# Performance work log

Hardware: AMD Instinct MI355X
Metric: run time of the kernel (lower is better)

The kernel has to match this reference:

```python
import jax, jax.numpy as jnp
import numpy as np

N = 50000      # users
F_IN = 768     # input features
H = 128        # hidden_dimension == linear_channels
E = 400000     # edges per relation
SQRT_D = float(np.sqrt(H))  # heads=1 -> d = H


def leaky_relu(x):
    return jnp.where(x >= 0, x, 0.01 * x)


def hgt_layer(x, edge_list, Wk, bk, Wq, bq, Wv, bv, rel_params, Wa, ba, skip):
    # x: [N, H]; edge_list: list of [2, E] int arrays (row0=src, row1=dst)
    n = x.shape[0]
    k = x @ Wk + bk
    q = x @ Wq + bq
    v = x @ Wv + bv
    out = jnp.zeros_like(x)
    for ei, (A, M, p) in zip(edge_list, rel_params):
        src, dst = ei[0], ei[1]
        kr = (k @ A)[src]                                  # [E, H] gather
        vr = (v @ M)[src]                                  # [E, H] gather
        alpha = jnp.sum(q[dst] * kr, axis=-1) * p[0] / SQRT_D  # [E]
        amax = jax.ops.segment_max(alpha, dst, num_segments=n)
        ex = jnp.exp(alpha - amax[dst])
        denom = jax.ops.segment_sum(ex, dst, num_segments=n)
        w = ex / denom[dst]                                # segment softmax per dst
        out = out + jax.ops.segment_sum(vr * w[:, None], dst, num_segments=n)
    out = jax.nn.gelu(out, approximate=False) @ Wa + ba
    beta = jax.nn.sigmoid(skip[0])                          # learnable skip gate
    return beta * out + (1.0 - beta) * x


def setup_inputs() -> dict:
    key = jax.random.key(0)
    ks = jax.random.split(key, 16)
    d = {}
    d['features'] = jax.random.normal(ks[0], (N, F_IN), dtype=jnp.float32)
    d['edge_index0'] = jax.random.randint(ks[1], (2, E), 0, N, dtype=jnp.int64)
    d['edge_index1'] = jax.random.randint(ks[2], (2, E), 0, N, dtype=jnp.int64)
    d['W1'] = jax.random.normal(ks[3], (F_IN, H), dtype=jnp.float32) / np.sqrt(F_IN)
    d['b1'] = jnp.zeros((H,), jnp.float32)
    d['Wk'] = jax.random.normal(ks[4], (H, H), dtype=jnp.float32) / np.sqrt(H)
    d['bk'] = jnp.zeros((H,), jnp.float32)
    d['Wq'] = jax.random.normal(ks[5], (H, H), dtype=jnp.float32) / np.sqrt(H)
    d['bq'] = jnp.zeros((H,), jnp.float32)
    d['Wv'] = jax.random.normal(ks[6], (H, H), dtype=jnp.float32) / np.sqrt(H)
    d['bv'] = jnp.zeros((H,), jnp.float32)
    d['A0'] = jax.random.normal(ks[7], (H, H), dtype=jnp.float32) / np.sqrt(H)
    d['M0'] = jax.random.normal(ks[8], (H, H), dtype=jnp.float32) / np.sqrt(H)
    d['p0'] = jnp.ones((1,), jnp.float32)
    d['A1'] = jax.random.normal(ks[9], (H, H), dtype=jnp.float32) / np.sqrt(H)
    d['M1'] = jax.random.normal(ks[10], (H, H), dtype=jnp.float32) / np.sqrt(H)
    d['p1'] = jnp.ones((1,), jnp.float32)
    d['Wa'] = jax.random.normal(ks[11], (H, H), dtype=jnp.float32) / np.sqrt(H)
    d['ba'] = jnp.zeros((H,), jnp.float32)
    d['skip'] = jnp.ones((1,), jnp.float32)
    d['Wo1'] = jax.random.normal(ks[12], (H, 64), dtype=jnp.float32) / np.sqrt(H)
    d['bo1'] = jnp.zeros((64,), jnp.float32)
    d['Wo2'] = jax.random.normal(ks[13], (64, 2), dtype=jnp.float32) / np.sqrt(64)
    d['bo2'] = jnp.zeros((2,), jnp.float32)
    return d


def reference(features, edge_index0, edge_index1, W1, b1, Wk, bk, Wq, bq, Wv, bv,
              A0, M0, p0, A1, M1, p1, Wa, ba, skip, Wo1, bo1, Wo2, bo2):
    edges = [edge_index0, edge_index1]
    rel_params = [(A0, M0, p0), (A1, M1, p1)]
    # linear1 + LeakyReLU (dropout is identity in eval mode)
    x = leaky_relu(features @ W1 + b1)
    # HGT_layer1 applied twice (as in the original forward)
    x = hgt_layer(x, edges, Wk, bk, Wq, bq, Wv, bv, rel_params, Wa, ba, skip)
    x = hgt_layer(x, edges, Wk, bk, Wq, bq, Wv, bv, rel_params, Wa, ba, skip)
    x = leaky_relu(x @ Wo1 + bo1)
    return x @ Wo2 + bo2
```

## Files before the change

### kernel.cpp

```cpp
#include <hip/hip_runtime.h>
#include <math.h>

#define NNODES 50000
#define FIN 768
#define HDIM 128
#define NEDGE 400000
#define NSB 49

typedef _Float16 half8 __attribute__((ext_vector_type(8)));
typedef _Float16 half4 __attribute__((ext_vector_type(4)));
typedef _Float16 half2v __attribute__((ext_vector_type(2)));
typedef float f32x4 __attribute__((ext_vector_type(4)));

__device__ __forceinline__ void gld_lds16(const void* g, void* l) {
    __builtin_amdgcn_global_load_lds((const __attribute__((address_space(1))) unsigned int*)g,
                                     (__attribute__((address_space(3))) unsigned int*)l, 16, 0, 0);
}


__global__ __launch_bounds__(256) void count2_kernel(const int* __restrict__ ei0, const int* __restrict__ ei1,
                                                     int* __restrict__ deg0, int* __restrict__ deg1) {
    int e = blockIdx.x * 256 + threadIdx.x;
    const int* ei = blockIdx.y ? ei1 : ei0;
    int* deg = blockIdx.y ? deg1 : deg0;
    if (e < NEDGE) atomicAdd(&deg[ei[NEDGE + e]], 1);
}

__global__ __launch_bounds__(1024) void scan1_kernel(const int* __restrict__ deg0, const int* __restrict__ deg1,
                                                     int* __restrict__ ptr0, int* __restrict__ ptr1,
                                                     int* __restrict__ sums) {
    const int r = blockIdx.y;
    const int* deg = r ? deg1 : deg0;
    int* ptr = r ? ptr1 : ptr0;
    const int b = blockIdx.x, t = threadIdx.x, i = b * 1024 + t;
    __shared__ int buf[1024];
    int v = (i < NNODES) ? deg[i] : 0;
    buf[t] = v;
    __syncthreads();
    for (int off = 1; off < 1024; off <<= 1) {
        int x = (t >= off) ? buf[t - off] : 0;
        __syncthreads();
        buf[t] += x;
        __syncthreads();
    }
    if (i < NNODES) ptr[i] = buf[t] - v;
    if (t == 1023) sums[r * 64 + b] = buf[1023];
}

__global__ __launch_bounds__(64) void scan2_kernel(int* __restrict__ sums,
                                                   int* __restrict__ ptr0, int* __restrict__ ptr1) {
    const int r = blockIdx.x, t = threadIdx.x;
    int orig = (t < NSB) ? sums[r * 64 + t] : 0;
    int v = orig;
    #pragma unroll
    for (int off = 1; off < 64; off <<= 1) {
        int u = __shfl_up(v, off, 64);
        if (t >= off) v += u;
    }
    if (t < NSB) sums[r * 64 + t] = v - orig;
    if (t == NSB - 1) (r ? ptr1 : ptr0)[NNODES] = v;
}

__global__ __launch_bounds__(1024) void scan3_kernel(const int* __restrict__ sums,
                                                     int* __restrict__ ptr0, int* __restrict__ ptr1) {
    const int r = blockIdx.y;
    int* ptr = r ? ptr1 : ptr0;
    const int i = blockIdx.x * 1024 + threadIdx.x;
    if (i < NNODES) ptr[i] += sums[r * 64 + blockIdx.x];
}

__global__ __launch_bounds__(256) void scatter2_kernel(const int* __restrict__ ei0, const int* __restrict__ ei1,
                                                       const int* __restrict__ ptr0, const int* __restrict__ ptr1,
                                                       int* __restrict__ fill0, int* __restrict__ fill1,
                                                       int* __restrict__ csr0, int* __restrict__ csr1) {
    int e = blockIdx.x * 256 + threadIdx.x;
    const int* ei = blockIdx.y ? ei1 : ei0;
    const int* ptr = blockIdx.y ? ptr1 : ptr0;
    int* fill = blockIdx.y ? fill1 : fill0;
    int* csr = blockIdx.y ? csr1 : csr0;
    if (e < NEDGE) {
        int s = ei[e], d = ei[NEDGE + e];
        int p = atomicAdd(&fill[d], 1);
        csr[ptr[d] + p] = s;
    }
}

__global__ __launch_bounds__(256) void gemm_cmb_kernel(
    const float* __restrict__ Wk, const float* __restrict__ Wv,
    const float* __restrict__ A0v, const float* __restrict__ M0v,
    const float* __restrict__ A1v, const float* __restrict__ M1v,
    float* __restrict__ WkA0, float* __restrict__ WvM0,
    float* __restrict__ WkA1, float* __restrict__ WvM1)
{
    const int z = blockIdx.z;
    const float* A = (z & 1) ? Wv : Wk;
    const float* B = (z == 0) ? A0v : (z == 1) ? M0v : (z == 2) ? A1v : M1v;
    float* C = (z == 0) ? WkA0 : (z == 1) ? WvM0 : (z == 2) ? WkA1 : WvM1;
    const int M = 128, N = 128, K = 128;
    __shared__ float As[16][64];
    __shared__ float Bs[16][64];
    const int t = threadIdx.x;
    const int tx = t & 15, ty = t >> 4;
    const int bm = blockIdx.x * 64, bn = blockIdx.y * 64;
    const int ar = t >> 2, ac = (t & 3) << 2;
    const int br = t >> 4, bc = (t & 15) << 2;
    float acc[4][4] = {};
    for (int kb = 0; kb < K; kb += 16) {
        float4 av = *reinterpret_cast<const float4*>(A + (size_t)(bm + ar) * K + kb + ac);
        float4 bv = *reinterpret_cast<const float4*>(B + (size_t)(kb + br) * N + bn + bc);
        __syncthreads();
        As[ac + 0][ar] = av.x; As[ac + 1][ar] = av.y; As[ac + 2][ar] = av.z; As[ac + 3][ar] = av.w;
        *reinterpret_cast<float4*>(&Bs[br][bc]) = bv;
        __syncthreads();
        #pragma unroll
        for (int kk = 0; kk < 16; ++kk) {
            float4 a = *reinterpret_cast<const float4*>(&As[kk][ty << 2]);
            float4 b = *reinterpret_cast<const float4*>(&Bs[kk][tx << 2]);
            float am[4] = {a.x, a.y, a.z, a.w};
            float bb[4] = {b.x, b.y, b.z, b.w};
            #pragma unroll
            for (int i = 0; i < 4; ++i)
                #pragma unroll
                for (int j = 0; j < 4; ++j)
                    acc[i][j] = fmaf(am[i], bb[j], acc[i][j]);
        }
    }
    #pragma unroll
    for (int i = 0; i < 4; ++i)
        #pragma unroll
        for (int j = 0; j < 4; ++j)
            C[(size_t)(bm + (ty << 2) + i) * N + bn + (tx << 2) + j] = acc[i][j];
}

__global__ __launch_bounds__(128) void bias_cmb_kernel(
    const float* __restrict__ bk, const float* __restrict__ bv,
    const float* __restrict__ A0v, const float* __restrict__ M0v,
    const float* __restrict__ A1v, const float* __restrict__ M1v,
    float* __restrict__ bqkv)
{
    const int z = blockIdx.x;
    const int j = threadIdx.x;
    const float* b = (z & 1) ? bv : bk;
    const float* Mtx = (z == 0) ? A0v : (z == 1) ? M0v : (z == 2) ? A1v : M1v;
    float s = 0.f;
    for (int i = 0; i < HDIM; ++i) s += b[i] * Mtx[i * HDIM + j];
    const int r = z >> 1, kv = z & 1;
    bqkv[128 + r * 256 + ((j >> 1) << 2) + (kv << 1) + (j & 1)] = s;
}

__global__ __launch_bounds__(128) void pack_qkvT(
    const float* __restrict__ Wq,   const float* __restrict__ WkA0, const float* __restrict__ WvM0,
    const float* __restrict__ WkA1, const float* __restrict__ WvM1,
    const float* __restrict__ bq,
    _Float16* __restrict__ WT, float* __restrict__ bb)
{
    int n = blockIdx.x;
    int k = threadIdx.x;
    int seg = n >> 7, col = n & 127;
    const float* W = (seg == 0) ? Wq : (seg == 1) ? WkA0 : (seg == 2) ? WvM0 : (seg == 3) ? WkA1 : WvM1;
    int np;
    if (seg == 0) np = col;
    else {
        int r = (seg - 1) >> 1, kv = (seg - 1) & 1;
        np = 128 + r * 256 + ((col >> 1) << 2) + (kv << 1) + (col & 1);
    }
    WT[(size_t)np * 128 + k] = (_Float16)W[(size_t)k * 128 + col];
    if (seg == 0 && k == 0) bb[col] = bq[col];
}

__global__ void transpose_h(const float* __restrict__ W, _Float16* __restrict__ WT, int K, int N) {
    int n = blockIdx.x, k = threadIdx.x;
    WT[(size_t)n * K + k] = (_Float16)W[(size_t)k * N + n];
}

template<int MODE, bool A_F32, bool GELU>
__global__ __launch_bounds__(256) void gemm_h(
    const void* __restrict__ Av, const _Float16* __restrict__ Bt,
    const float* __restrict__ bias, const _Float16* __restrict__ Dh,
    const float* __restrict__ gate, _Float16* __restrict__ C,
    int M, int N, int K)
{
    __shared__ _Float16 sA[4096];
    __shared__ _Float16 sB[4096];
    const int t = threadIdx.x;
    const int w = t >> 6, lane = t & 63;
    const int wm = w >> 1, wn = w & 1;
    const int bm = blockIdx.x * 128, bn = blockIdx.y * 128;
    const f32x4 zero = {0.f, 0.f, 0.f, 0.f};
    f32x4 acc[4][4];
    #pragma unroll
    for (int i = 0; i < 4; ++i)
        #pragma unroll
        for (int j = 0; j < 4; ++j) acc[i][j] = zero;

    for (int kb = 0; kb < K; kb += 32) {
        #pragma unroll
        for (int it = 0; it < 2; ++it) {
            const int c = it * 256 + t;
            const int l = c & 63;
            const int row = ((c >> 6) << 4) | (l & 15);
            const int kc = (l >> 4) << 3;
            const int cb = it * 256 + (t & 192);
            int arow = bm + row; if (arow > M - 1) arow = M - 1;
            int brow = bn + row; if (brow > N - 1) brow = N - 1;
            if (A_F32) {
                const float* ap = (const float*)Av + (size_t)arow * K + kb + kc;
                f32x4 v0 = *(const f32x4*)ap;
                f32x4 v1 = *(const f32x4*)(ap + 4);
                float tmp[8] = {v0[0], v0[1], v0[2], v0[3], v1[0], v1[1], v1[2], v1[3]};
                half8 av;
                #pragma unroll
                for (int j = 0; j < 8; ++j) {
                    float x = tmp[j];
                    if (GELU) x = 0.5f * x * (1.0f + erff(x * 0.70710678118654752f));
                    av[j] = (_Float16)x;
                }
                *(half8*)(sA + (size_t)c * 8) = av;
            } else {
                gld_lds16((const _Float16*)Av + (size_t)arow * K + kb + kc, sA + (size_t)cb * 8);
            }
            gld_lds16(Bt + (size_t)brow * K + kb + kc, sB + (size_t)cb * 8);
        }
        __syncthreads();
        half8 af[4], bf[4];
        #pragma unroll
        for (int i = 0; i < 4; ++i) af[i] = *(const half8*)(sA + ((size_t)((wm * 4 + i) * 64 + lane)) * 8);
        #pragma unroll
        for (int i = 0; i < 4; ++i) bf[i] = *(const half8*)(sB + ((size_t)((wn * 4 + i) * 64 + lane)) * 8);
        #pragma unroll
        for (int i = 0; i < 4; ++i)
            #pragma unroll
            for (int j = 0; j < 4; ++j)
                acc[i][j] = __builtin_amdgcn_mfma_f32_16x16x32_f16(af[i], bf[j], acc[i][j], 0, 0, 0);
        __syncthreads();
    }

    float be = 0.f;
    if (MODE == 2) be = 1.0f / (1.0f + __expf(-gate[0]));
    const int crow0 = bm + wm * 64;
    const int ccol0 = bn + wn * 64;
    #pragma unroll
    for (int i = 0; i < 4; ++i) {
        #pragma unroll
        for (int j = 0; j < 4; ++j) {
            const int col = ccol0 + j * 16 + (lane & 15);
            if (col >= N) continue;
            #pragma unroll
            for (int r = 0; r < 4; ++r) {
                const int row = crow0 + i * 16 + ((lane >> 4) << 2) + r;
                if (row >= M) continue;
                float val = acc[i][j][r] + bias[col];
                if (MODE == 1) val = (val >= 0.f) ? val : 0.01f * val;
                if (MODE == 2) val = be * val + (1.f - be) * (float)Dh[(size_t)row * HDIM + col];
                C[(size_t)row * N + col] = (_Float16)val;
            }
        }
    }
}

template<int MODE, bool A_F32, bool GELU>
__global__ __launch_bounds__(256) void gemm_h32(
    const void* __restrict__ Av, const _Float16* __restrict__ Bt,
    const float* __restrict__ bias, const _Float16* __restrict__ Dh,
    const float* __restrict__ gate, _Float16* __restrict__ C,
    int M, int N, int K)
{
    __shared__ _Float16 sA[4 * 64 * 8];
    __shared__ _Float16 sB[16 * 64 * 8];
    const int t = threadIdx.x;
    const int w = t >> 6, lane = t & 63;
    const int rl = lane & 15, kg = lane >> 4;
    const int bm = blockIdx.x * 32;
    const f32x4 zero = {0.f, 0.f, 0.f, 0.f};
    f32x4 acc[2][2] = {{zero, zero}, {zero, zero}};

    for (int kb = 0; kb < K; kb += 64) {
        {
            const int mi = w >> 1, kk = w & 1;
            int arow = bm + mi * 16 + rl; if (arow > M - 1) arow = M - 1;
            const int ko = kb + kk * 32 + kg * 8;
            if (A_F32) {
                const float* ap = (const float*)Av + (size_t)arow * K + ko;
                f32x4 v0 = *(const f32x4*)ap;
                f32x4 v1 = *(const f32x4*)(ap + 4);
                float tmp[8] = {v0[0], v0[1], v0[2], v0[3], v1[0], v1[1], v1[2], v1[3]};
                half8 av;
                #pragma unroll
                for (int j = 0; j < 8; ++j) {
                    float x = tmp[j];
                    if (GELU) x = 0.5f * x * (1.0f + erff(x * 0.70710678118654752f));
                    av[j] = (_Float16)x;
                }
                *(half8*)(sA + (size_t)(w * 64 + lane) * 8) = av;
            } else {
                gld_lds16((const _Float16*)Av + (size_t)arow * K + ko, sA + (size_t)(w * 64) * 8);
            }
        }
        #pragma unroll
        for (int j = 0; j < 4; ++j) {
            const int fb = w * 4 + j;
            const int ni = (j >> 1) & 1, kk = j & 1;
            int nrow = w * 32 + ni * 16 + rl; if (nrow > N - 1) nrow = N - 1;
            gld_lds16(Bt + (size_t)nrow * K + kb + kk * 32 + kg * 8, sB + (size_t)(fb * 64) * 8);
        }
        __syncthreads();
        half8 af[2][2], bf[2][2];
        #pragma unroll
        for (int mi = 0; mi < 2; ++mi)
            #pragma unroll
            for (int kk = 0; kk < 2; ++kk)
                af[mi][kk] = *(const half8*)(sA + (size_t)((mi * 2 + kk) * 64 + lane) * 8);
        #pragma unroll
        for (int ni = 0; ni < 2; ++ni)
            #pragma unroll
            for (int kk = 0; kk < 2; ++kk)
                bf[ni][kk] = *(const half8*)(sB + (size_t)((w * 4 + ni * 2 + kk) * 64 + lane) * 8);
        #pragma unroll
        for (int mi = 0; mi < 2; ++mi)
            #pragma unroll
            for (int ni = 0; ni < 2; ++ni)
                #pragma unroll
                for (int kk = 0; kk < 2; ++kk)
                    acc[mi][ni] = __builtin_amdgcn_mfma_f32_16x16x32_f16(af[mi][kk], bf[ni][kk], acc[mi][ni], 0, 0, 0);
        __syncthreads();
    }

    float be = 0.f;
    if (MODE == 2) be = 1.0f / (1.0f + __expf(-gate[0]));
    #pragma unroll
    for (int mi = 0; mi < 2; ++mi) {
        #pragma unroll
        for (int ni = 0; ni < 2; ++ni) {
            const int col = w * 32 + ni * 16 + rl;
            if (col >= N) continue;
            #pragma unroll
            for (int r = 0; r < 4; ++r) {
                const int row = bm + mi * 16 + kg * 4 + r;
                if (row >= M) continue;
                float val = acc[mi][ni][r] + bias[col];
                if (MODE == 1) val = (val >= 0.f) ? val : 0.01f * val;
                if (MODE == 2) val = be * val + (1.f - be) * (float)Dh[(size_t)row * HDIM + col];
                C[(size_t)row * N + col] = (_Float16)val;
            }
        }
    }
}

__global__ __launch_bounds__(256) void attn2_kernel(
    const _Float16* __restrict__ qkv,
    const int* __restrict__ ptr0, const int* __restrict__ csr0,
    const int* __restrict__ ptr1, const int* __restrict__ csr1,
    const float* __restrict__ p0, const float* __restrict__ p1,
    float* __restrict__ att)
{
    const int w = (blockIdx.x * 256 + threadIdx.x) >> 6;
    if (w >= NNODES) return;
    const int lane = threadIdx.x & 63;
    half2v qh = *(const half2v*)(qkv + (size_t)w * 640 + (lane << 1));
    const float qx = (float)qh[0], qy = (float)qh[1];
    float ox = 0.f, oy = 0.f;
    #pragma unroll
    for (int r = 0; r < 2; ++r) {
        const int* ptrv = r ? ptr1 : ptr0;
        const int* csr  = r ? csr1 : csr0;
        const float scale = (r ? p1[0] : p0[0]) * 0.08838834764831845f;
        const int start = ptrv[w], end = ptrv[w + 1];
        if (start == end) continue;
        const _Float16* tbl = qkv + 128 + 256 * r + (lane << 2);
        float denom = 0.f, ax = 0.f, ay = 0.f;
        int i = start;
        for (; i + 4 <= end; i += 4) {
            const int s0 = csr[i], s1 = csr[i + 1], s2 = csr[i + 2], s3 = csr[i + 3];
            half4 kv0 = *(const half4*)(tbl + (size_t)s0 * 640);
            half4 kv1 = *(const half4*)(tbl + (size_t)s1 * 640);
            half4 kv2 = *(const half4*)(tbl + (size_t)s2 * 640);
            half4 kv3 = *(const half4*)(tbl + (size_t)s3 * 640);
            float d0 = qx * (float)kv0[0] + qy * (float)kv0[1];
            float d1 = qx * (float)kv1[0] + qy * (float)kv1[1];
            float d2 = qx * (float)kv2[0] + qy * (float)kv2[1];
            float d3 = qx * (float)kv3[0] + qy * (float)kv3[1];
            #pragma unroll
            for (int o2 = 32; o2; o2 >>= 1) {
                d0 += __shfl_xor(d0, o2, 64);
                d1 += __shfl_xor(d1, o2, 64);
                d2 += __shfl_xor(d2, o2, 64);
                d3 += __shfl_xor(d3, o2, 64);
            }
            const float e0 = __expf(d0 * scale), e1 = __expf(d1 * scale);
            const float e2 = __expf(d2 * scale), e3 = __expf(d3 * scale);
            denom += (e0 + e1) + (e2 + e3);
            ax += e0 * (float)kv0[2] + e1 * (float)kv1[2] + e2 * (float)kv2[2] + e3 * (float)kv3[2];
            ay += e0 * (float)kv0[3] + e1 * (float)kv1[3] + e2 * (float)kv2[3] + e3 * (float)kv3[3];
        }
        for (; i < end; ++i) {
            const int s = csr[i];
            half4 kv = *(const half4*)(tbl + (size_t)s * 640);
            float d = qx * (float)kv[0] + qy * (float)kv[1];
            #pragma unroll
            for (int o2 = 32; o2; o2 >>= 1) d += __shfl_xor(d, o2, 64);
            const float e = __expf(d * scale);
            denom += e;
            ax += e * (float)kv[2];
            ay += e * (float)kv[3];
        }
        const float inv = 1.0f / denom;
        ox += ax * inv; oy += ay * inv;
    }
    *reinterpret_cast<float2*>(att + (size_t)w * HDIM + (lane << 1)) = make_float2(ox, oy);
}

__global__ __launch_bounds__(256) void head2_kernel(const _Float16* __restrict__ h,
                                                    const float* __restrict__ Wo2,
                                                    const float* __restrict__ bo2,
                                                    float* __restrict__ out)
{
    int i = blockIdx.x * 256 + threadIdx.x;
    if (i >= NNODES) return;
    const _Float16* hp = h + (size_t)i * 64;
    float s0 = bo2[0], s1 = bo2[1];
    #pragma unroll
    for (int j0 = 0; j0 < 64; j0 += 8) {
        half8 hv = *(const half8*)(hp + j0);
        #pragma unroll
        for (int j = 0; j < 8; ++j) {
            float v = (float)hv[j];
            s0 += v * Wo2[2 * (j0 + j)];
            s1 += v * Wo2[2 * (j0 + j) + 1];
        }
    }
    out[2 * i] = s0;
    out[2 * i + 1] = s1;
}


extern "C" void kernel_launch(void* const* d_in, const int* in_sizes, int n_in,
                              void* d_out, int out_size, void* d_ws, size_t ws_size,
                              hipStream_t stream)
{
    const float* features = (const float*)d_in[0];
    const int* ei0 = (const int*)d_in[1];
    const int* ei1 = (const int*)d_in[2];
    const float* W1 = (const float*)d_in[3];
    const float* b1 = (const float*)d_in[4];
    const float* Wk = (const float*)d_in[5];
    const float* bk = (const float*)d_in[6];
    const float* Wq = (const float*)d_in[7];
    const float* bq = (const float*)d_in[8];
    const float* Wv = (const float*)d_in[9];
    const float* bv = (const float*)d_in[10];
    const float* A0 = (const float*)d_in[11];
    const float* M0 = (const float*)d_in[12];
    const float* p0 = (const float*)d_in[13];
    const float* A1 = (const float*)d_in[14];
    const float* M1 = (const float*)d_in[15];
    const float* p1 = (const float*)d_in[16];
    const float* Wa = (const float*)d_in[17];
    const float* ba = (const float*)d_in[18];
    const float* skip = (const float*)d_in[19];
    const float* Wo1 = (const float*)d_in[20];
    const float* bo1 = (const float*)d_in[21];
    const float* Wo2 = (const float*)d_in[22];
    const float* bo2 = (const float*)d_in[23];
    (void)in_sizes; (void)n_in; (void)out_size; (void)ws_size;

    char* base = (char*)d_ws;
    size_t off = 0;
    auto alloc = [&](size_t bytes) { size_t r = off; off = (off + bytes + 255) & ~(size_t)255; return base + r; };

    _Float16* x0h  = (_Float16*)alloc((size_t)NNODES * HDIM * 2);
    _Float16* x1h  = (_Float16*)alloc((size_t)NNODES * HDIM * 2);
    _Float16* qkv  = (_Float16*)alloc((size_t)NNODES * 640 * 2);
    float*    att  = (float*)   alloc((size_t)NNODES * HDIM * 4);
    _Float16* hh   = (_Float16*)alloc((size_t)NNODES * 64 * 2);
    float* WkA[2]  = { (float*)alloc(65536), (float*)alloc(65536) };
    float* WvM[2]  = { (float*)alloc(65536), (float*)alloc(65536) };
    _Float16* WqkvT = (_Float16*)alloc(640 * 128 * 2);
    float*    bqkv  = (float*)   alloc(640 * 4);
    _Float16* W1T   = (_Float16*)alloc(128 * 768 * 2);
    _Float16* WaT   = (_Float16*)alloc(128 * 128 * 2);
    _Float16* Wo1T  = (_Float16*)alloc(64 * 128 * 2);
    int* deg[2]  = { (int*)alloc(NNODES * 4), (int*)alloc(NNODES * 4) };
    int* ptrv[2] = { (int*)alloc((NNODES + 1) * 4), (int*)alloc((NNODES + 1) * 4) };
    int* fill[2] = { (int*)alloc(NNODES * 4), (int*)alloc(NNODES * 4) };
    int* csr[2]  = { (int*)alloc(NEDGE * 4),  (int*)alloc(NEDGE * 4) };
    int* sums    = (int*)alloc(2 * 64 * 4);

    hipMemsetAsync(deg[0], 0, NNODES * 4, stream);
    hipMemsetAsync(deg[1], 0, NNODES * 4, stream);
    hipMemsetAsync(fill[0], 0, NNODES * 4, stream);
    hipMemsetAsync(fill[1], 0, NNODES * 4, stream);
    const int egrid = (NEDGE + 255) / 256;
    count2_kernel<<<dim3(egrid, 2), 256, 0, stream>>>(ei0, ei1, deg[0], deg[1]);
    scan1_kernel<<<dim3(NSB, 2), 1024, 0, stream>>>(deg[0], deg[1], ptrv[0], ptrv[1], sums);
    scan2_kernel<<<2, 64, 0, stream>>>(sums, ptrv[0], ptrv[1]);
    scan3_kernel<<<dim3(NSB, 2), 1024, 0, stream>>>(sums, ptrv[0], ptrv[1]);
    scatter2_kernel<<<dim3(egrid, 2), 256, 0, stream>>>(ei0, ei1, ptrv[0], ptrv[1],
                                                        fill[0], fill[1], csr[0], csr[1]);

    gemm_cmb_kernel<<<dim3(2, 2, 4), 256, 0, stream>>>(Wk, Wv, A0, M0, A1, M1,
                                                       WkA[0], WvM[0], WkA[1], WvM[1]);
    bias_cmb_kernel<<<4, 128, 0, stream>>>(bk, bv, A0, M0, A1, M1, bqkv);

    pack_qkvT<<<640, 128, 0, stream>>>(Wq, WkA[0], WvM[0], WkA[1], WvM[1], bq, WqkvT, bqkv);
    transpose_h<<<128, 768, 0, stream>>>(W1, W1T, 768, 128);
    transpose_h<<<128, 128, 0, stream>>>(Wa, WaT, 128, 128);
    transpose_h<<<64, 128, 0, stream>>>(Wo1, Wo1T, 128, 64);

    const int MBLK = (NNODES + 127) / 128;
    const int MBLK32 = (NNODES + 31) / 32;

    gemm_h32<1, true, false><<<MBLK32, 256, 0, stream>>>(
        features, W1T, b1, nullptr, nullptr, x0h, NNODES, HDIM, FIN);

    _Float16* xin = x0h;
    _Float16* xout = x1h;
    for (int layer = 0; layer < 2; ++layer) {
        gemm_h<0, false, false><<<dim3(MBLK, 5), 256, 0, stream>>>(
            xin, WqkvT, bqkv, nullptr, nullptr, qkv, NNODES, 640, HDIM);
        attn2_kernel<<<(NNODES * 64 + 255) / 256, 256, 0, stream>>>(
            qkv, ptrv[0], csr[0], ptrv[1], csr[1], p0, p1, att);
        gemm_h32<2, true, true><<<MBLK32, 256, 0, stream>>>(
            att, WaT, ba, xin, skip, xout, NNODES, HDIM, HDIM);
        _Float16* tmp = xin; xin = xout; xout = tmp;
    }

    gemm_h32<1, false, false><<<MBLK32, 256, 0, stream>>>(
        xin, Wo1T, bo1, nullptr, nullptr, hh, NNODES, 64, HDIM);
    head2_kernel<<<(NNODES + 255) / 256, 256, 0, stream>>>(hh, Wo2, bo2, (float*)d_out);
}
```

Measured before the change: 482.3 us.

## Double-buffer LDS tiles in GEMM kernels to overlap loads with MFMA

Both GEMM kernels now keep two LDS buffers. The loads for the next K tile are issued before the MFMAs on the current tile, and only one barrier runs per iteration. For fp32 A inputs the values are held in registers across the MFMA block and converted (with optional GELU) into the other buffer afterwards. This is meant to hide global-load latency behind compute, at the cost of double the LDS footprint and more live registers, which may lower occupancy.

New measurement: 495.1 us. 2.7% more time.

```diff
diff --git a/kernel.cpp b/kernel.cpp
--- a/kernel.cpp
+++ b/kernel.cpp
@@ -15,6 +15,19 @@
 __device__ __forceinline__ void gld_lds16(const void* g, void* l) {
     __builtin_amdgcn_global_load_lds((const __attribute__((address_space(1))) unsigned int*)g,
                                      (__attribute__((address_space(3))) unsigned int*)l, 16, 0, 0);
+}
+
+template<bool GELU>
+__device__ __forceinline__ void cvt_store(_Float16* dst, f32x4 v0, f32x4 v1) {
+    float tmp[8] = {v0[0], v0[1], v0[2], v0[3], v1[0], v1[1], v1[2], v1[3]};
+    half8 av;
+    #pragma unroll
+    for (int j = 0; j < 8; ++j) {
+        float x = tmp[j];
+        if (GELU) x = 0.5f * x * (1.0f + erff(x * 0.70710678118654752f));
+        av[j] = (_Float16)x;
+    }
+    *(half8*)dst = av;
 }
 
 
@@ -180,12 +193,29 @@
     const float* __restrict__ gate, _Float16* __restrict__ C,
     int M, int N, int K)
 {
-    __shared__ _Float16 sA[4096];
-    __shared__ _Float16 sB[4096];
-    const int t = threadIdx.x;
-    const int w = t >> 6, lane = t & 63;
+    __shared__ _Float16 sA[2][4096];
+    __shared__ _Float16 sB[2][4096];
+    const int tid = threadIdx.x;
+    const int w = tid >> 6, lane = tid & 63;
     const int wm = w >> 1, wn = w & 1;
     const int bm = blockIdx.x * 128, bn = blockIdx.y * 128;
+
+    int arow0, arow1, brow0, brow1, kc0, kc1, cb0, cb1, c0, c1;
+    {
+        const int c = tid, l = c & 63;
+        const int row = ((c >> 6) << 4) | (l & 15);
+        kc0 = (l >> 4) << 3; cb0 = (tid & 192); c0 = c;
+        arow0 = bm + row; if (arow0 > M - 1) arow0 = M - 1;
+        brow0 = bn + row; if (brow0 > N - 1) brow0 = N - 1;
+    }
+    {
+        const int c = 256 + tid, l = c & 63;
+        const int row = ((c >> 6) << 4) | (l & 15);
+        kc1 = (l >> 4) << 3; cb1 = 256 + (tid & 192); c1 = c;
+        arow1 = bm + row; if (arow1 > M - 1) arow1 = M - 1;
+        brow1 = bn + row; if (brow1 > N - 1) brow1 = N - 1;
+    }
+
     const f32x4 zero = {0.f, 0.f, 0.f, 0.f};
     f32x4 acc[4][4];
     #pragma unroll
@@ -193,46 +223,60 @@
         #pragma unroll
         for (int j = 0; j < 4; ++j) acc[i][j] = zero;
 
-    for (int kb = 0; kb < K; kb += 32) {
-        #pragma unroll
-        for (int it = 0; it < 2; ++it) {
-            const int c = it * 256 + t;
-            const int l = c & 63;
-            const int row = ((c >> 6) << 4) | (l & 15);
-            const int kc = (l >> 4) << 3;
-            const int cb = it * 256 + (t & 192);
-            int arow = bm + row; if (arow > M - 1) arow = M - 1;
-            int brow = bn + row; if (brow > N - 1) brow = N - 1;
+    const int nt = K >> 5;
+    f32x4 pa00, pa01, pa10, pa11;
+
+    if (A_F32) {
+        const float* a0 = (const float*)Av + (size_t)arow0 * K + kc0;
+        pa00 = *(const f32x4*)a0; pa01 = *(const f32x4*)(a0 + 4);
+        const float* a1 = (const float*)Av + (size_t)arow1 * K + kc1;
+        pa10 = *(const f32x4*)a1; pa11 = *(const f32x4*)(a1 + 4);
+    } else {
+        gld_lds16((const _Float16*)Av + (size_t)arow0 * K + kc0, sA[0] + (size_t)cb0 * 8);
+        gld_lds16((const _Float16*)Av + (size_t)arow1 * K + kc1, sA[0] + (size_t)cb1 * 8);
+    }
+    gld_lds16(Bt + (size_t)brow0 * K + kc0, sB[0] + (size_t)cb0 * 8);
+    gld_lds16(Bt + (size_t)brow1 * K + kc1, sB[0] + (size_t)cb1 * 8);
+    if (A_F32) {
+        cvt_store<GELU>(sA[0] + (size_t)c0 * 8, pa00, pa01);
+        cvt_store<GELU>(sA[0] + (size_t)c1 * 8, pa10, pa11);
+    }
+    __syncthreads();
+
+    int buf = 0;
+    for (int t = 0; t < nt; ++t) {
+        const int nxt = buf ^ 1;
+        const bool more = (t + 1) < nt;
+        if (more) {
+            const int kb = (t + 1) << 5;
             if (A_F32) {
-                const float* ap = (const float*)Av + (size_t)arow * K + kb + kc;
-                f32x4 v0 = *(const f32x4*)ap;
-                f32x4 v1 = *(const f32x4*)(ap + 4);
-                float tmp[8] = {v0[0], v0[1], v0[2], v0[3], v1[0], v1[1], v1[2], v1[3]};
-                half8 av;
-                #pragma unroll
-                for (int j = 0; j < 8; ++j) {
-                    float x = tmp[j];
-                    if (GELU) x = 0.5f * x * (1.0f + erff(x * 0.70710678118654752f));
-                    av[j] = (_Float16)x;
-                }
-                *(half8*)(sA + (size_t)c * 8) = av;
+                const float* a0 = (const float*)Av + (size_t)arow0 * K + kb + kc0;
+                pa00 = *(const f32x4*)a0; pa01 = *(const f32x4*)(a0 + 4);
+                const float* a1 = (const float*)Av + (size_t)arow1 * K + kb + kc1;
+                pa10 = *(const f32x4*)a1; pa11 = *(const f32x4*)(a1 + 4);
             } else {
-                gld_lds16((const _Float16*)Av + (size_t)arow * K + kb + kc, sA + (size_t)cb * 8);
+                gld_lds16((const _Float16*)Av + (size_t)arow0 * K + kb + kc0, sA[nxt] + (size_t)cb0 * 8);
+                gld_lds16((const _Float16*)Av + (size_t)arow1 * K + kb + kc1, sA[nxt] + (size_t)cb1 * 8);
             }
-            gld_lds16(Bt + (size_t)brow * K + kb + kc, sB + (size_t)cb * 8);
-        }
-        __syncthreads();
+            gld_lds16(Bt + (size_t)brow0 * K + kb + kc0, sB[nxt] + (size_t)cb0 * 8);
+            gld_lds16(Bt + (size_t)brow1 * K + kb + kc1, sB[nxt] + (size_t)cb1 * 8);
+        }
         half8 af[4], bf[4];
         #pragma unroll
-        for (int i = 0; i < 4; ++i) af[i] = *(const half8*)(sA + ((size_t)((wm * 4 + i) * 64 + lane)) * 8);
-        #pragma unroll
-        for (int i = 0; i < 4; ++i) bf[i] = *(const half8*)(sB + ((size_t)((wn * 4 + i) * 64 + lane)) * 8);
+        for (int i = 0; i < 4; ++i) af[i] = *(const half8*)(sA[buf] + ((size_t)((wm * 4 + i) * 64 + lane)) * 8);
+        #pragma unroll
+        for (int i = 0; i < 4; ++i) bf[i] = *(const half8*)(sB[buf] + ((size_t)((wn * 4 + i) * 64 + lane)) * 8);
         #pragma unroll
         for (int i = 0; i < 4; ++i)
             #pragma unroll
             for (int j = 0; j < 4; ++j)
                 acc[i][j] = __builtin_amdgcn_mfma_f32_16x16x32_f16(af[i], bf[j], acc[i][j], 0, 0, 0);
+        if (more && A_F32) {
+            cvt_store<GELU>(sA[nxt] + (size_t)c0 * 8, pa00, pa01);
+            cvt_store<GELU>(sA[nxt] + (size_t)c1 * 8, pa10, pa11);
+        }
         __syncthreads();
+        buf = nxt;
     }
 
     float be = 0.f;
@@ -265,79 +309,93 @@
     const float* __restrict__ gate, _Float16* __restrict__ C,
     int M, int N, int K)
 {
-    __shared__ _Float16 sA[4 * 64 * 8];
-    __shared__ _Float16 sB[16 * 64 * 8];
-    const int t = threadIdx.x;
-    const int w = t >> 6, lane = t & 63;
+    __shared__ _Float16 sA[2][4 * 64 * 8];
+    __shared__ _Float16 sB[2][16 * 64 * 8];
+    const int tid = threadIdx.x;
+    const int w = tid >> 6, lane = tid & 63;
     const int rl = lane & 15, kg = lane >> 4;
     const int bm = blockIdx.x * 32;
     const f32x4 zero = {0.f, 0.f, 0.f, 0.f};
     f32x4 acc[2][2] = {{zero, zero}, {zero, zero}};
 
-    for (int kb = 0; kb < K; kb += 64) {
-        {
-            const int mi = w >> 1, kk = w & 1;
-            int arow = bm + mi * 16 + rl; if (arow > M - 1) arow = M - 1;
-            const int ko = kb + kk * 32 + kg * 8;
+    const int mi = w >> 1, kkA = w & 1;
+    int arow = bm + mi * 16 + rl; if (arow > M - 1) arow = M - 1;
+    const int koA = kkA * 32 + kg * 8;
+    int nrowB[4];
+    #pragma unroll
+    for (int j = 0; j < 4; ++j) {
+        const int ni = (j >> 1) & 1;
+        int nr = w * 32 + ni * 16 + rl; if (nr > N - 1) nr = N - 1;
+        nrowB[j] = nr;
+    }
+
+    const int nt = K >> 6;
+    f32x4 pv0, pv1;
+
+    if (A_F32) {
+        const float* ap = (const float*)Av + (size_t)arow * K + koA;
+        pv0 = *(const f32x4*)ap; pv1 = *(const f32x4*)(ap + 4);
+    } else {
+        gld_lds16((const _Float16*)Av + (size_t)arow * K + koA, sA[0] + (size_t)(w * 64) * 8);
+    }
+    #pragma unroll
+    for (int j = 0; j < 4; ++j)
+        gld_lds16(Bt + (size_t)nrowB[j] * K + (j & 1) * 32 + kg * 8, sB[0] + (size_t)((w * 4 + j) * 64) * 8);
+    if (A_F32) cvt_store<GELU>(sA[0] + (size_t)(w * 64 + lane) * 8, pv0, pv1);
+    __syncthreads();
+
+    int buf = 0;
+    for (int t = 0; t < nt; ++t) {
+        const int nxt = buf ^ 1;
+        const bool more = (t + 1) < nt;
+        if (more) {
+            const int kb = (t + 1) << 6;
             if (A_F32) {
-                const float* ap = (const float*)Av + (size_t)arow * K + ko;
-                f32x4 v0 = *(const f32x4*)ap;
-                f32x4 v1 = *(const f32x4*)(ap + 4);
-                float tmp[8] = {v0[0], v0[1], v0[2], v0[3], v1[0], v1[1], v1[2], v1[3]};
-                half8 av;
-                #pragma unroll
-                for (int j = 0; j < 8; ++j) {
-                    float x = tmp[j];
-                    if (GELU) x = 0.5f * x * (1.0f + erff(x * 0.70710678118654752f));
-                    av[j] = (_Float16)x;
-                }
-                *(half8*)(sA + (size_t)(w * 64 + lane) * 8) = av;
+                const float* ap = (const float*)Av + (size_t)arow * K + kb + koA;
+                pv0 = *(const f32x4*)ap; pv1 = *(const f32x4*)(ap + 4);
             } else {
-                gld_lds16((const _Float16*)Av + (size_t)arow * K + ko, sA + (size_t)(w * 64) * 8);
+                gld_lds16((const _Float16*)Av + (size_t)arow * K + kb + koA, sA[nxt] + (size_t)(w * 64) * 8);
             }
-        }
-        #pragma unroll
-        for (int j = 0; j < 4; ++j) {
-            const int fb = w * 4 + j;
-            const int ni = (j >> 1) & 1, kk = j & 1;
-            int nrow = w * 32 + ni * 16 + rl; if (nrow > N - 1) nrow = N - 1;
-            gld_lds16(Bt + (size_t)nrow * K + kb + kk * 32 + kg * 8, sB + (size_t)(fb * 64) * 8);
-        }
-        __syncthreads();
+            #pragma unroll
+            for (int j = 0; j < 4; ++j)
+                gld_lds16(Bt + (size_t)nrowB[j] * K + kb + (j & 1) * 32 + kg * 8, sB[nxt] + (size_t)((w * 4 + j) * 64) * 8);
+        }
         half8 af[2][2], bf[2][2];
         #pragma unroll
-        for (int mi = 0; mi < 2; ++mi)
+        for (int mi2 = 0; mi2 < 2; ++mi2)
             #pragma unroll
             for (int kk = 0; kk < 2; ++kk)
-                af[mi][kk] = *(const half8*)(sA + (size_t)((mi * 2 + kk) * 64 + lane) * 8);
+                af[mi2][kk] = *(const half8*)(sA[buf] + (size_t)((mi2 * 2 + kk) * 64 + lane) * 8);
         #pragma unroll
         for (int ni = 0; ni < 2; ++ni)
             #pragma unroll
             for (int kk = 0; kk < 2; ++kk)
-                bf[ni][kk] = *(const half8*)(sB + (size_t)((w * 4 + ni * 2 + kk) * 64 + lane) * 8);
-        #pragma unroll
-        for (int mi = 0; mi < 2; ++mi)
+                bf[ni][kk] = *(const half8*)(sB[buf] + (size_t)((w * 4 + ni * 2 + kk) * 64 + lane) * 8);
+        #pragma unroll
+        for (int mi2 = 0; mi2 < 2; ++mi2)
             #pragma unroll
             for (int ni = 0; ni < 2; ++ni)
                 #pragma unroll
                 for (int kk = 0; kk < 2; ++kk)
-                    acc[mi][ni] = __builtin_amdgcn_mfma_f32_16x16x32_f16(af[mi][kk], bf[ni][kk], acc[mi][ni], 0, 0, 0);
+                    acc[mi2][ni] = __builtin_amdgcn_mfma_f32_16x16x32_f16(af[mi2][kk], bf[ni][kk], acc[mi2][ni], 0, 0, 0);
+        if (more && A_F32) cvt_store<GELU>(sA[nxt] + (size_t)(w * 64 + lane) * 8, pv0, pv1);
         __syncthreads();
+        buf = nxt;
     }
 
     float be = 0.f;
     if (MODE == 2) be = 1.0f / (1.0f + __expf(-gate[0]));
     #pragma unroll
-    for (int mi = 0; mi < 2; ++mi) {
+    for (int mi2 = 0; mi2 < 2; ++mi2) {
         #pragma unroll
         for (int ni = 0; ni < 2; ++ni) {
             const int col = w * 32 + ni * 16 + rl;
             if (col >= N) continue;
             #pragma unroll
             for (int r = 0; r < 4; ++r) {
-                const int row = bm + mi * 16 + kg * 4 + r;
+                const int row = bm + mi2 * 16 + kg * 4 + r;
                 if (row >= M) continue;
-                float val = acc[mi][ni][r] + bias[col];
+                float val = acc[mi2][ni][r] + bias[col];
                 if (MODE == 1) val = (val >= 0.f) ? val : 0.01f * val;
                 if (MODE == 2) val = be * val + (1.f - be) * (float)Dh[(size_t)row * HDIM + col];
                 C[(size_t)row * N + col] = (_Float16)val;
```

## Restructure dense GEMMs: whole-K LDS staging and double-buffered feature GEMM

Applied to the files above, without the earlier changes.

Replaces the generic K-looped GEMM kernels with two specialised ones. The feature projection kernel now loads the whole 32x768 A tile into LDS once, converting it to fp16, and double-buffers the B tiles so the next weight load overlaps the MFMAs. The K=128 GEMMs (QKV, output projection with GELU/skip, Wo1) now stage all of K for a 128x128 tile in LDS up front with a single barrier, instead of looping over K with two syncs per step. The aim is fewer barriers and better overlap, at the cost of much larger LDS per block and possibly lower occupancy; the Wa and Wo1 GEMMs also move from 32-row to 128-row tiles, which gives fewer blocks.

Measured after the change: 532.5 us. +10.4%, slower.

```diff
diff --git a/kernel.cpp b/kernel.cpp
--- a/kernel.cpp
+++ b/kernel.cpp
@@ -6,6 +6,7 @@
 #define HDIM 128
 #define NEDGE 400000
 #define NSB 49
+#define FKT 12
 
 typedef _Float16 half8 __attribute__((ext_vector_type(8)));
 typedef _Float16 half4 __attribute__((ext_vector_type(4)));
@@ -15,6 +16,18 @@
 __device__ __forceinline__ void gld_lds16(const void* g, void* l) {
     __builtin_amdgcn_global_load_lds((const __attribute__((address_space(1))) unsigned int*)g,
                                      (__attribute__((address_space(3))) unsigned int*)l, 16, 0, 0);
+}
+
+template<bool GELU>
+__device__ __forceinline__ half8 cvt8(f32x4 v0, f32x4 v1) {
+    half8 av;
+    #pragma unroll
+    for (int j = 0; j < 8; ++j) {
+        float x = (j < 4) ? v0[j] : v1[j - 4];
+        if (GELU) x = 0.5f * x * (1.0f + erff(x * 0.70710678118654752f));
+        av[j] = (_Float16)x;
+    }
+    return av;
 }
 
 
@@ -96,7 +109,7 @@
     const float* A = (z & 1) ? Wv : Wk;
     const float* B = (z == 0) ? A0v : (z == 1) ? M0v : (z == 2) ? A1v : M1v;
     float* C = (z == 0) ? WkA0 : (z == 1) ? WvM0 : (z == 2) ? WkA1 : WvM1;
-    const int M = 128, N = 128, K = 128;
+    const int N = 128, K = 128;
     __shared__ float As[16][64];
     __shared__ float Bs[16][64];
     const int t = threadIdx.x;
@@ -173,148 +186,65 @@
     WT[(size_t)n * K + k] = (_Float16)W[(size_t)k * N + n];
 }
 
-template<int MODE, bool A_F32, bool GELU>
-__global__ __launch_bounds__(256) void gemm_h(
-    const void* __restrict__ Av, const _Float16* __restrict__ Bt,
-    const float* __restrict__ bias, const _Float16* __restrict__ Dh,
-    const float* __restrict__ gate, _Float16* __restrict__ C,
-    int M, int N, int K)
-{
-    __shared__ _Float16 sA[4096];
-    __shared__ _Float16 sB[4096];
-    const int t = threadIdx.x;
-    const int w = t >> 6, lane = t & 63;
-    const int wm = w >> 1, wn = w & 1;
-    const int bm = blockIdx.x * 128, bn = blockIdx.y * 128;
-    const f32x4 zero = {0.f, 0.f, 0.f, 0.f};
-    f32x4 acc[4][4];
-    #pragma unroll
-    for (int i = 0; i < 4; ++i)
-        #pragma unroll
-        for (int j = 0; j < 4; ++j) acc[i][j] = zero;
-
-    for (int kb = 0; kb < K; kb += 32) {
-        #pragma unroll
-        for (int it = 0; it < 2; ++it) {
-            const int c = it * 256 + t;
-            const int l = c & 63;
-            const int row = ((c >> 6) << 4) | (l & 15);
-            const int kc = (l >> 4) << 3;
-            const int cb = it * 256 + (t & 192);
-            int arow = bm + row; if (arow > M - 1) arow = M - 1;
-            int brow = bn + row; if (brow > N - 1) brow = N - 1;
-            if (A_F32) {
-                const float* ap = (const float*)Av + (size_t)arow * K + kb + kc;
-                f32x4 v0 = *(const f32x4*)ap;
-                f32x4 v1 = *(const f32x4*)(ap + 4);
-                float tmp[8] = {v0[0], v0[1], v0[2], v0[3], v1[0], v1[1], v1[2], v1[3]};
-                half8 av;
-                #pragma unroll
-                for (int j = 0; j < 8; ++j) {
-                    float x = tmp[j];
-                    if (GELU) x = 0.5f * x * (1.0f + erff(x * 0.70710678118654752f));
-                    av[j] = (_Float16)x;
-                }
-                *(half8*)(sA + (size_t)c * 8) = av;
-            } else {
-                gld_lds16((const _Float16*)Av + (size_t)arow * K + kb + kc, sA + (size_t)cb * 8);
-            }
-            gld_lds16(Bt + (size_t)brow * K + kb + kc, sB + (size_t)cb * 8);
-        }
-        __syncthreads();
-        half8 af[4], bf[4];
-        #pragma unroll
-        for (int i = 0; i < 4; ++i) af[i] = *(const half8*)(sA + ((size_t)((wm * 4 + i) * 64 + lane)) * 8);
-        #pragma unroll
-        for (int i = 0; i < 4; ++i) bf[i] = *(const half8*)(sB + ((size_t)((wn * 4 + i) * 64 + lane)) * 8);
-        #pragma unroll
-        for (int i = 0; i < 4; ++i)
-            #pragma unroll
-            for (int j = 0; j < 4; ++j)
-                acc[i][j] = __builtin_amdgcn_mfma_f32_16x16x32_f16(af[i], bf[j], acc[i][j], 0, 0, 0);
-        __syncthreads();
-    }
-
-    float be = 0.f;
-    if (MODE == 2) be = 1.0f / (1.0f + __expf(-gate[0]));
-    const int crow0 = bm + wm * 64;
-    const int ccol0 = bn + wn * 64;
-    #pragma unroll
-    for (int i = 0; i < 4; ++i) {
-        #pragma unroll
-        for (int j = 0; j < 4; ++j) {
-            const int col = ccol0 + j * 16 + (lane & 15);
-            if (col >= N) continue;
-            #pragma unroll
-            for (int r = 0; r < 4; ++r) {
-                const int row = crow0 + i * 16 + ((lane >> 4) << 2) + r;
-                if (row >= M) continue;
-                float val = acc[i][j][r] + bias[col];
-                if (MODE == 1) val = (val >= 0.f) ? val : 0.01f * val;
-                if (MODE == 2) val = be * val + (1.f - be) * (float)Dh[(size_t)row * HDIM + col];
-                C[(size_t)row * N + col] = (_Float16)val;
-            }
-        }
-    }
-}
-
-template<int MODE, bool A_F32, bool GELU>
-__global__ __launch_bounds__(256) void gemm_h32(
-    const void* __restrict__ Av, const _Float16* __restrict__ Bt,
-    const float* __restrict__ bias, const _Float16* __restrict__ Dh,
-    const float* __restrict__ gate, _Float16* __restrict__ C,
-    int M, int N, int K)
-{
-    __shared__ _Float16 sA[4 * 64 * 8];
-    __shared__ _Float16 sB[16 * 64 * 8];
+__global__ __launch_bounds__(256) void gemm_feat(
+    const float* __restrict__ A, const _Float16* __restrict__ Bt,
+    const float* __restrict__ bias, _Float16* __restrict__ C)
+{
+    __shared__ _Float16 sA[FKT * 4 * 64 * 8];
+    __shared__ _Float16 sB[2][16 * 64 * 8];
     const int t = threadIdx.x;
     const int w = t >> 6, lane = t & 63;
     const int rl = lane & 15, kg = lane >> 4;
     const int bm = blockIdx.x * 32;
+    const int M = NNODES;
+
+    #pragma unroll
+    for (int r = 0; r < FKT; ++r) {
+        const int c = r * 256 + t;
+        const int kt = c >> 8;
+        const int cc = c & 255;
+        const int fa = cc >> 6;
+        const int l  = cc & 63;
+        const int row = ((fa >> 1) << 4) + (l & 15);
+        const int k = kt * 64 + ((fa & 1) << 5) + ((l >> 4) << 3);
+        int arow = bm + row; if (arow > M - 1) arow = M - 1;
+        const float* ap = A + (size_t)arow * FIN + k;
+        f32x4 v0 = *(const f32x4*)ap;
+        f32x4 v1 = *(const f32x4*)(ap + 4);
+        *(half8*)(sA + (size_t)c * 8) = cvt8<false>(v0, v1);
+    }
+
+    int nrow[4];
+    #pragma unroll
+    for (int j = 0; j < 4; ++j) nrow[j] = w * 32 + (((j >> 1) & 1) << 4) + rl;
+    #pragma unroll
+    for (int j = 0; j < 4; ++j)
+        gld_lds16(Bt + (size_t)nrow[j] * FIN + ((j & 1) << 5) + (kg << 3),
+                  sB[0] + (size_t)((w * 4 + j) * 64) * 8);
+    __syncthreads();
+
     const f32x4 zero = {0.f, 0.f, 0.f, 0.f};
     f32x4 acc[2][2] = {{zero, zero}, {zero, zero}};
-
-    for (int kb = 0; kb < K; kb += 64) {
-        {
-            const int mi = w >> 1, kk = w & 1;
-            int arow = bm + mi * 16 + rl; if (arow > M - 1) arow = M - 1;
-            const int ko = kb + kk * 32 + kg * 8;
-            if (A_F32) {
-                const float* ap = (const float*)Av + (size_t)arow * K + ko;
-                f32x4 v0 = *(const f32x4*)ap;
-                f32x4 v1 = *(const f32x4*)(ap + 4);
-                float tmp[8] = {v0[0], v0[1], v0[2], v0[3], v1[0], v1[1], v1[2], v1[3]};
-                half8 av;
-                #pragma unroll
-                for (int j = 0; j < 8; ++j) {
-                    float x = tmp[j];
-                    if (GELU) x = 0.5f * x * (1.0f + erff(x * 0.70710678118654752f));
-                    av[j] = (_Float16)x;
-                }
-                *(half8*)(sA + (size_t)(w * 64 + lane) * 8) = av;
-            } else {
-                gld_lds16((const _Float16*)Av + (size_t)arow * K + ko, sA + (size_t)(w * 64) * 8);
-            }
-        }
-        #pragma unroll
-        for (int j = 0; j < 4; ++j) {
-            const int fb = w * 4 + j;
-            const int ni = (j >> 1) & 1, kk = j & 1;
-            int nrow = w * 32 + ni * 16 + rl; if (nrow > N - 1) nrow = N - 1;
-            gld_lds16(Bt + (size_t)nrow * K + kb + kk * 32 + kg * 8, sB + (size_t)(fb * 64) * 8);
-        }
-        __syncthreads();
+    int buf = 0;
+    for (int kt = 0; kt < FKT; ++kt) {
+        if (kt + 1 < FKT) {
+            const int kb = (kt + 1) << 6;
+            #pragma unroll
+            for (int j = 0; j < 4; ++j)
+                gld_lds16(Bt + (size_t)nrow[j] * FIN + kb + ((j & 1) << 5) + (kg << 3),
+                          sB[buf ^ 1] + (size_t)((w * 4 + j) * 64) * 8);
+        }
         half8 af[2][2], bf[2][2];
         #pragma unroll
         for (int mi = 0; mi < 2; ++mi)
             #pragma unroll
             for (int kk = 0; kk < 2; ++kk)
-                af[mi][kk] = *(const half8*)(sA + (size_t)((mi * 2 + kk) * 64 + lane) * 8);
+                af[mi][kk] = *(const half8*)(sA + (size_t)(((kt * 4 + mi * 2 + kk) * 64) + lane) * 8);
         #pragma unroll
         for (int ni = 0; ni < 2; ++ni)
             #pragma unroll
             for (int kk = 0; kk < 2; ++kk)
-                bf[ni][kk] = *(const half8*)(sB + (size_t)((w * 4 + ni * 2 + kk) * 64 + lane) * 8);
+                bf[ni][kk] = *(const half8*)(sB[buf] + (size_t)(((w * 4 + ni * 2 + kk) * 64) + lane) * 8);
         #pragma unroll
         for (int mi = 0; mi < 2; ++mi)
             #pragma unroll
@@ -323,21 +253,108 @@
                 for (int kk = 0; kk < 2; ++kk)
                     acc[mi][ni] = __builtin_amdgcn_mfma_f32_16x16x32_f16(af[mi][kk], bf[ni][kk], acc[mi][ni], 0, 0, 0);
         __syncthreads();
-    }
-
-    float be = 0.f;
-    if (MODE == 2) be = 1.0f / (1.0f + __expf(-gate[0]));
+        buf ^= 1;
+    }
+
     #pragma unroll
     for (int mi = 0; mi < 2; ++mi) {
         #pragma unroll
         for (int ni = 0; ni < 2; ++ni) {
             const int col = w * 32 + ni * 16 + rl;
-            if (col >= N) continue;
             #pragma unroll
             for (int r = 0; r < 4; ++r) {
                 const int row = bm + mi * 16 + kg * 4 + r;
                 if (row >= M) continue;
                 float val = acc[mi][ni][r] + bias[col];
+                val = (val >= 0.f) ? val : 0.01f * val;
+                C[(size_t)row * HDIM + col] = (_Float16)val;
+            }
+        }
+    }
+}
+
+template<int MODE, bool A_F32, bool GELU>
+__global__ __launch_bounds__(256) void gemm_t128(
+    const void* __restrict__ Av, const _Float16* __restrict__ Bt,
+    const float* __restrict__ bias, const _Float16* __restrict__ Dh,
+    const float* __restrict__ gate, _Float16* __restrict__ C,
+    int M, int N)
+{
+    const int K = 128;
+    __shared__ _Float16 sA[4 * 8 * 64 * 8];
+    __shared__ _Float16 sB[4 * 8 * 64 * 8];
+    const int t = threadIdx.x;
+    const int w = t >> 6, lane = t & 63;
+    const int wm = w >> 1, wn = w & 1;
+    const int bm = blockIdx.x * 128, bn = blockIdx.y * 128;
+
+    #pragma unroll
+    for (int r = 0; r < 8; ++r) {
+        const int c = r * 256 + t;
+        const int kt = c >> 9;
+        const int f  = (c >> 6) & 7;
+        const int l  = c & 63;
+        const int row = f * 16 + (l & 15);
+        const int k = kt * 32 + ((l >> 4) << 3);
+        int arow = bm + row; if (arow > M - 1) arow = M - 1;
+        if (A_F32) {
+            const float* ap = (const float*)Av + (size_t)arow * K + k;
+            f32x4 v0 = *(const f32x4*)ap;
+            f32x4 v1 = *(const f32x4*)(ap + 4);
+            *(half8*)(sA + (size_t)c * 8) = cvt8<GELU>(v0, v1);
+        } else {
+            gld_lds16((const _Float16*)Av + (size_t)arow * K + k, sA + (size_t)(r * 256 + w * 64) * 8);
+        }
+    }
+    #pragma unroll
+    for (int r = 0; r < 8; ++r) {
+        const int c = r * 256 + t;
+        const int kt = c >> 9;
+        const int f  = (c >> 6) & 7;
+        const int l  = c & 63;
+        const int col = f * 16 + (l & 15);
+        const int k = kt * 32 + ((l >> 4) << 3);
+        int brow = bn + col; if (brow > N - 1) brow = N - 1;
+        gld_lds16(Bt + (size_t)brow * K + k, sB + (size_t)(r * 256 + w * 64) * 8);
+    }
+    __syncthreads();
+
+    const f32x4 zero = {0.f, 0.f, 0.f, 0.f};
+    f32x4 acc[4][4];
+    #pragma unroll
+    for (int i = 0; i < 4; ++i)
+        #pragma unroll
+        for (int j = 0; j < 4; ++j) acc[i][j] = zero;
+
+    #pragma unroll
+    for (int kt = 0; kt < 4; ++kt) {
+        half8 af[4], bf[4];
+        #pragma unroll
+        for (int i = 0; i < 4; ++i) af[i] = *(const half8*)(sA + (size_t)(((kt * 8 + wm * 4 + i) * 64) + lane) * 8);
+        #pragma unroll
+        for (int i = 0; i < 4; ++i) bf[i] = *(const half8*)(sB + (size_t)(((kt * 8 + wn * 4 + i) * 64) + lane) * 8);
+        #pragma unroll
+        for (int i = 0; i < 4; ++i)
+            #pragma unroll
+            for (int j = 0; j < 4; ++j)
+                acc[i][j] = __builtin_amdgcn_mfma_f32_16x16x32_f16(af[i], bf[j], acc[i][j], 0, 0, 0);
+    }
+
+    float be = 0.f;
+    if (MODE == 2) be = 1.0f / (1.0f + __expf(-gate[0]));
+    const int crow0 = bm + wm * 64;
+    const int ccol0 = bn + wn * 64;
+    #pragma unroll
+    for (int i = 0; i < 4; ++i) {
+        #pragma unroll
+        for (int j = 0; j < 4; ++j) {
+            const int col = ccol0 + j * 16 + (lane & 15);
+            if (col >= N) continue;
+            #pragma unroll
+            for (int r = 0; r < 4; ++r) {
+                const int row = crow0 + i * 16 + ((lane >> 4) << 2) + r;
+                if (row >= M) continue;
+                float val = acc[i][j][r] + bias[col];
                 if (MODE == 1) val = (val >= 0.f) ? val : 0.01f * val;
                 if (MODE == 2) val = be * val + (1.f - be) * (float)Dh[(size_t)row * HDIM + col];
                 C[(size_t)row * N + col] = (_Float16)val;
@@ -506,25 +523,24 @@
     transpose_h<<<128, 128, 0, stream>>>(Wa, WaT, 128, 128);
     transpose_h<<<64, 128, 0, stream>>>(Wo1, Wo1T, 128, 64);
 
-    const int MBLK = (NNODES + 127) / 128;
     const int MBLK32 = (NNODES + 31) / 32;
-
-    gemm_h32<1, true, false><<<MBLK32, 256, 0, stream>>>(
-        features, W1T, b1, nullptr, nullptr, x0h, NNODES, HDIM, FIN);
+    const int MBLK128 = (NNODES + 127) / 128;
+
+    gemm_feat<<<MBLK32, 256, 0, stream>>>(features, W1T, b1, x0h);
 
     _Float16* xin = x0h;
     _Float16* xout = x1h;
     for (int layer = 0; layer < 2; ++layer) {
-        gemm_h<0, false, false><<<dim3(MBLK, 5), 256, 0, stream>>>(
-            xin, WqkvT, bqkv, nullptr, nullptr, qkv, NNODES, 640, HDIM);
+        gemm_t128<0, false, false><<<dim3(MBLK128, 5), 256, 0, stream>>>(
+            xin, WqkvT, bqkv, nullptr, nullptr, qkv, NNODES, 640);
         attn2_kernel<<<(NNODES * 64 + 255) / 256, 256, 0, stream>>>(
             qkv, ptrv[0], csr[0], ptrv[1], csr[1], p0, p1, att);
-        gemm_h32<2, true, true><<<MBLK32, 256, 0, stream>>>(
-            att, WaT, ba, xin, skip, xout, NNODES, HDIM, HDIM);
+        gemm_t128<2, true, true><<<dim3(MBLK128, 1), 256, 0, stream>>>(
+            att, WaT, ba, xin, skip, xout, NNODES, 128);
         _Float16* tmp = xin; xin = xout; xout = tmp;
     }
 
-    gemm_h32<1, false, false><<<MBLK32, 256, 0, stream>>>(
-        xin, Wo1T, bo1, nullptr, nullptr, hh, NNODES, 64, HDIM);
+    gemm_t128<1, false, false><<<dim3(MBLK128, 1), 256, 0, stream>>>(
+        xin, Wo1T, bo1, nullptr, nullptr, hh, NNODES, 64);
     head2_kernel<<<(NNODES + 255) / 256, 256, 0, stream>>>(hh, Wo2, bo2, (float*)d_out);
 }
```
